# Optimization experiments

Hardware: AMD Instinct MI355X
Metric: run time of the kernel (lower is better)

Reference implementation:

```python
import jax, jax.numpy as jnp
import numpy as np

N_NODES = 50000
IN_CH = 128
OUT_CH = 64
N_EDGES = 800000
K_HOPS = 2


def setup_inputs() -> dict:
    key = jax.random.key(0)
    k1, k2, k3, k4 = jax.random.split(key, 4)
    x = jax.random.normal(k1, (N_NODES, IN_CH), dtype=jnp.float32)
    edge_index = jax.random.randint(k2, (2, N_EDGES), 0, N_NODES, dtype=jnp.int64)
    # SGC linear layer params (torch Linear default init approx)
    scale = 1.0 / np.sqrt(IN_CH)
    W = jax.random.uniform(k3, (IN_CH, OUT_CH), dtype=jnp.float32, minval=-scale, maxval=scale)
    b = jax.random.uniform(k4, (OUT_CH,), dtype=jnp.float32, minval=-scale, maxval=scale)
    return {"x": x, "edge_index": edge_index, "W": W, "b": b}


def _sgc_propagate(x, row, col, K):
    # GCN symmetric normalization with self-loops: S = D^-1/2 (A+I) D^-1/2
    n = x.shape[0]
    loop = jnp.arange(n, dtype=row.dtype)
    row = jnp.concatenate([row, loop])
    col = jnp.concatenate([col, loop])
    ones = jnp.ones(row.shape[0], dtype=x.dtype)
    deg = jax.ops.segment_sum(ones, col, num_segments=n)
    dinv = jnp.where(deg > 0, jax.lax.rsqrt(deg), 0.0)
    norm = dinv[row] * dinv[col]  # [E+N]
    for _ in range(K):
        # gather source features, weight, scatter-add to targets
        msg = norm[:, None] * x[row]  # [E+N, C]
        x = jax.ops.segment_sum(msg, col, num_segments=n)
    return x


def reference(x, edge_index, W, b):
    # Dropout is identity in eval mode (deterministic reference).
    row, col = edge_index[0], edge_index[1]
    h = _sgc_propagate(x, row, col, K_HOPS)  # [N, IN_CH]
    return h @ W + b  # [N, OUT_CH]
```

## Files before the change

kernel.cpp:

```cpp
#include <hip/hip_runtime.h>

#define N_NODES 50000
#define IN_CH   128
#define OUT_CH  64
#define N_EDGES 800000
#define NBINS   49
#define LBCAP   128
#define BINCAP  20000
#define PCAP    64
#define WT_STR  136


using short8  = __attribute__((ext_vector_type(8))) short;
using float4v = __attribute__((ext_vector_type(4))) float;

__device__ __forceinline__ unsigned int bpack(float a, float b) {
    unsigned int ua = __float_as_uint(a), ub = __float_as_uint(b);
    unsigned int ra = (ua + 0x7fffu + ((ua >> 16) & 1u)) >> 16;
    unsigned int rb = (ub + 0x7fffu + ((ub >> 16) & 1u)) & 0xffff0000u;
    return (ra & 0xffffu) | rb;
}

__global__ __launch_bounds__(256) void scatter_a(const int* __restrict__ row,
        const int* __restrict__ col, unsigned int* __restrict__ binbuf,
        int* __restrict__ gcur) {
    __shared__ unsigned int sbuf[NBINS][LBCAP];
    __shared__ int scnt[NBINS];
    __shared__ int sdst[NBINS];
    const int tid = threadIdx.x;
    for (int i = tid; i < NBINS; i += 256) scnt[i] = 0;
    __syncthreads();
    const int e0 = blockIdx.x * (N_EDGES / 256);
    for (int i = tid; i < N_EDGES / 256; i += 256) {
        int e = e0 + i;
        int s = row[e], t = col[e];
        int b = t >> 10;
        int pos = atomicAdd(&scnt[b], 1);
        if (pos < LBCAP)
            sbuf[b][pos] = ((unsigned)(t & 1023) << 16) | (unsigned)s;
    }
    __syncthreads();
    for (int b = tid; b < NBINS; b += 256) {
        int c = scnt[b]; if (c > LBCAP) c = LBCAP; scnt[b] = c;
        sdst[b] = atomicAdd(&gcur[b], c);
    }
    __syncthreads();
    for (int b = 0; b < NBINS; ++b) {
        int c = scnt[b], d = sdst[b];
        for (int i = tid; i < c; i += 256)
            binbuf[(size_t)b * BINCAP + d + i] = sbuf[b][i];
    }
}

__global__ __launch_bounds__(1024) void scatter_b(const unsigned int* __restrict__ binbuf,
        const int* __restrict__ gcur, unsigned short* __restrict__ esrc,
        unsigned char* __restrict__ fill8) {
    __shared__ int lcnt[1024];
    const int b  = blockIdx.x;
    const int t0 = b << 10;
    const int tid = threadIdx.x;
    lcnt[tid] = 0;
    __syncthreads();
    int cnt = gcur[b]; if (cnt > BINCAP) cnt = BINCAP;
    const unsigned int* src = binbuf + (size_t)b * BINCAP;
    for (int i = tid; i < cnt; i += 1024) {
        unsigned int e = src[i];
        int tl = e >> 16;
        int pos = atomicAdd(&lcnt[tl], 1);
        int t = t0 + tl;
        if (pos < PCAP && t < N_NODES)
            esrc[(size_t)pos * N_NODES + t] = (unsigned short)(e & 0xffffu);
    }
    __syncthreads();
    int t = t0 + tid;
    if (t < N_NODES) {
        int v = lcnt[tid]; if (v > PCAP) v = PCAP;
        fill8[t] = (unsigned char)v;
    }
}

__global__ __launch_bounds__(256) void gemm_mfma(const float* __restrict__ x,
        const float* __restrict__ W, float* __restrict__ y) {
    __shared__ unsigned short sWT[64 * WT_STR];
    const int tid = threadIdx.x;
    for (int i = tid; i < IN_CH * OUT_CH; i += 256) {
        int k = i >> 6, c = i & 63;
        unsigned int u = __float_as_uint(W[i]);
        u = (u + 0x7fffu + ((u >> 16) & 1u)) >> 16;
        sWT[c * WT_STR + k] = (unsigned short)u;
    }
    __syncthreads();
    const int lane = tid & 63;
    const int quad = lane >> 4;
    const int c15  = lane & 15;

    short8 bf[4][4];
    #pragma unroll
    for (int t = 0; t < 4; ++t)
        #pragma unroll
        for (int ch = 0; ch < 4; ++ch)
            bf[ch][t] = *(const short8*)&sWT[(t * 16 + c15) * WT_STR + ch * 32 + quad * 8];

    const int wave = (blockIdx.x * 256 + tid) >> 6;
    for (int tile = wave; tile < N_NODES / 16; tile += 1024) {
        const float* xr = x + ((size_t)tile * 16 + c15) * IN_CH;
        float4v acc[4] = {{0.f,0.f,0.f,0.f},{0.f,0.f,0.f,0.f},
                          {0.f,0.f,0.f,0.f},{0.f,0.f,0.f,0.f}};
        #pragma unroll
        for (int ch = 0; ch < 4; ++ch) {
            float4 f0 = *(const float4*)(xr + ch * 32 + quad * 8);
            float4 f1 = *(const float4*)(xr + ch * 32 + quad * 8 + 4);
            unsigned int d0 = bpack(f0.x, f0.y), d1 = bpack(f0.z, f0.w);
            unsigned int d2 = bpack(f1.x, f1.y), d3 = bpack(f1.z, f1.w);
            short8 a;
            a[0] = (short)d0; a[1] = (short)(d0 >> 16);
            a[2] = (short)d1; a[3] = (short)(d1 >> 16);
            a[4] = (short)d2; a[5] = (short)(d2 >> 16);
            a[6] = (short)d3; a[7] = (short)(d3 >> 16);
            #pragma unroll
            for (int t = 0; t < 4; ++t)
                acc[t] = __builtin_amdgcn_mfma_f32_16x16x32_bf16(a, bf[ch][t], acc[t], 0, 0, 0);
        }
        #pragma unroll
        for (int t = 0; t < 4; ++t)
            #pragma unroll
            for (int r = 0; r < 4; ++r)
                y[((size_t)tile * 16 + quad * 4 + r) * OUT_CH + t * 16 + c15] = acc[t][r];
    }
}

__global__ __launch_bounds__(256) void scale_z0(const float* __restrict__ y,
        const unsigned char* __restrict__ fill8, uint4* __restrict__ z0) {
    int gid = blockIdx.x * 256 + threadIdx.x;
    if (gid >= N_NODES * 8) return;
    int n = gid >> 3, q = gid & 7;
    float d = rsqrtf((float)((int)fill8[n] + 1));
    float4 a = ((const float4*)y)[n * 16 + q * 2];
    float4 b = ((const float4*)y)[n * 16 + q * 2 + 1];
    uint4 pk;
    pk.x = bpack(d * a.x, d * a.y);
    pk.y = bpack(d * a.z, d * a.w);
    pk.z = bpack(d * b.x, d * b.y);
    pk.w = bpack(d * b.z, d * b.w);
    z0[gid] = pk;
}

__global__ __launch_bounds__(256) void hop_gather(const uint4* __restrict__ hin,
        void* __restrict__ hout, const unsigned char* __restrict__ fill8,
        const unsigned short* __restrict__ esrc, const float* __restrict__ bias,
        int last) {
    int lane = threadIdx.x & 63;
    int g = lane >> 3;
    int q = lane & 7;
    int t = __builtin_amdgcn_readfirstlane(blockIdx.x * 4 + (threadIdx.x >> 6));
    if (t >= N_NODES) return;
    int deg = fill8[t];

    float acc[8] = {};
    if (g == 0) {
        uint4 r = hin[t * 8 + q];
        const unsigned int rw[4] = { r.x, r.y, r.z, r.w };
        #pragma unroll
        for (int j = 0; j < 4; ++j) {
            acc[2 * j]     = __uint_as_float(rw[j] << 16);
            acc[2 * j + 1] = __uint_as_float(rw[j] & 0xffff0000u);
        }
    }
    for (int base = 0; base < deg; base += 8) {
        int e = base + g;
        if (e < deg) {
            int s = (int)esrc[(size_t)e * N_NODES + t];
            uint4 r = hin[s * 8 + q];
            const unsigned int rw[4] = { r.x, r.y, r.z, r.w };
            #pragma unroll
            for (int j = 0; j < 4; ++j) {
                acc[2 * j]     += __uint_as_float(rw[j] << 16);
                acc[2 * j + 1] += __uint_as_float(rw[j] & 0xffff0000u);
            }
        }
    }
    #pragma unroll
    for (int j = 0; j < 8; ++j) {
        acc[j] += __shfl_xor(acc[j], 8);
        acc[j] += __shfl_xor(acc[j], 16);
        acc[j] += __shfl_xor(acc[j], 32);
    }
    if (g == 0) {
        if (!last) {
            float rdeg = 1.0f / (float)(deg + 1);
            uint4 pk;
            pk.x = bpack(acc[0] * rdeg, acc[1] * rdeg);
            pk.y = bpack(acc[2] * rdeg, acc[3] * rdeg);
            pk.z = bpack(acc[4] * rdeg, acc[5] * rdeg);
            pk.w = bpack(acc[6] * rdeg, acc[7] * rdeg);
            ((uint4*)hout)[t * 8 + q] = pk;
        } else {
            float d = rsqrtf((float)(deg + 1));
            float4 b0 = ((const float4*)bias)[q * 2];
            float4 b1 = ((const float4*)bias)[q * 2 + 1];
            float4 o0 = make_float4(d * acc[0] + b0.x, d * acc[1] + b0.y,
                                    d * acc[2] + b0.z, d * acc[3] + b0.w);
            float4 o1 = make_float4(d * acc[4] + b1.x, d * acc[5] + b1.y,
                                    d * acc[6] + b1.z, d * acc[7] + b1.w);
            ((float4*)hout)[t * 16 + q * 2]     = o0;
            ((float4*)hout)[t * 16 + q * 2 + 1] = o1;
        }
    }
}

extern "C" void kernel_launch(void* const* d_in, const int* in_sizes, int n_in,
                              void* d_out, int out_size, void* d_ws, size_t ws_size,
                              hipStream_t stream) {
    const float* x  = (const float*)d_in[0];
    const int*   ei = (const int*)d_in[1];
    const float* W  = (const float*)d_in[2];
    const float* b  = (const float*)d_in[3];
    float*       out = (float*)d_out;

    const int* row = ei;
    const int* col = ei + N_EDGES;

    char* ws = (char*)d_ws;
    size_t a = 0;
    auto alloc = [&](size_t bytes) { char* p = ws + a; a = (a + bytes + 255) & ~(size_t)255; return p; };
    int*            gcur   = (int*)           alloc(NBINS * sizeof(int));
    unsigned int*   binbuf = (unsigned int*)  alloc((size_t)NBINS * BINCAP * 4);
    unsigned short* esrc   = (unsigned short*)alloc((size_t)PCAP * N_NODES * 2);
    unsigned char*  fill8  = (unsigned char*) alloc(N_NODES);
    float*          y      = (float*)         alloc((size_t)N_NODES * OUT_CH * 4);
    unsigned int*   z0     = (unsigned int*)  alloc((size_t)N_NODES * OUT_CH * 2);
    unsigned int*   z1     = (unsigned int*)  alloc((size_t)N_NODES * OUT_CH * 2);

    hipMemsetAsync(gcur, 0, NBINS * sizeof(int), stream);

    const int B = 256;
    int gS = (N_NODES * 8 + B - 1) / B;
    int gH = (N_NODES + 3) / 4;

    scatter_a<<<256, B, 0, stream>>>(row, col, binbuf, gcur);
    scatter_b<<<NBINS, 1024, 0, stream>>>(binbuf, gcur, esrc, fill8);
    gemm_mfma<<<256, B, 0, stream>>>(x, W, y);
    scale_z0 <<<gS, B, 0, stream>>>(y, fill8, (uint4*)z0);
    hop_gather<<<gH, B, 0, stream>>>((const uint4*)z0, (void*)z1, fill8, esrc, b, 0);
    hop_gather<<<gH, B, 0, stream>>>((const uint4*)z1, (void*)out, fill8, esrc, b, 1);
}
```

Measured before the change: 183.5 us.

## Merge bin scatter and GEMM into one launch and widen edge binning grid

```diff
diff --git a/kernel.cpp b/kernel.cpp
--- a/kernel.cpp
+++ b/kernel.cpp
@@ -9,6 +9,10 @@
 #define BINCAP  20000
 #define PCAP    64
 #define WT_STR  136
+#define SA_B    500
+#define SA_E    1600
+#define SB_B    49
+#define GEMM_BL 196
 
 
 using short8  = __attribute__((ext_vector_type(8))) short;
@@ -28,62 +32,69 @@
     __shared__ int scnt[NBINS];
     __shared__ int sdst[NBINS];
     const int tid = threadIdx.x;
-    for (int i = tid; i < NBINS; i += 256) scnt[i] = 0;
-    __syncthreads();
-    const int e0 = blockIdx.x * (N_EDGES / 256);
-    for (int i = tid; i < N_EDGES / 256; i += 256) {
-        int e = e0 + i;
-        int s = row[e], t = col[e];
-        int b = t >> 10;
-        int pos = atomicAdd(&scnt[b], 1);
-        if (pos < LBCAP)
-            sbuf[b][pos] = ((unsigned)(t & 1023) << 16) | (unsigned)s;
-    }
-    __syncthreads();
-    for (int b = tid; b < NBINS; b += 256) {
-        int c = scnt[b]; if (c > LBCAP) c = LBCAP; scnt[b] = c;
-        sdst[b] = atomicAdd(&gcur[b], c);
-    }
-    __syncthreads();
-    for (int b = 0; b < NBINS; ++b) {
-        int c = scnt[b], d = sdst[b];
-        for (int i = tid; i < c; i += 256)
-            binbuf[(size_t)b * BINCAP + d + i] = sbuf[b][i];
-    }
-}
-
-__global__ __launch_bounds__(1024) void scatter_b(const unsigned int* __restrict__ binbuf,
-        const int* __restrict__ gcur, unsigned short* __restrict__ esrc,
-        unsigned char* __restrict__ fill8) {
-    __shared__ int lcnt[1024];
-    const int b  = blockIdx.x;
-    const int t0 = b << 10;
-    const int tid = threadIdx.x;
-    lcnt[tid] = 0;
-    __syncthreads();
-    int cnt = gcur[b]; if (cnt > BINCAP) cnt = BINCAP;
-    const unsigned int* src = binbuf + (size_t)b * BINCAP;
-    for (int i = tid; i < cnt; i += 1024) {
-        unsigned int e = src[i];
-        int tl = e >> 16;
-        int pos = atomicAdd(&lcnt[tl], 1);
-        int t = t0 + tl;
-        if (pos < PCAP && t < N_NODES)
-            esrc[(size_t)pos * N_NODES + t] = (unsigned short)(e & 0xffffu);
-    }
-    __syncthreads();
-    int t = t0 + tid;
-    if (t < N_NODES) {
-        int v = lcnt[tid]; if (v > PCAP) v = PCAP;
-        fill8[t] = (unsigned char)v;
-    }
-}
-
-__global__ __launch_bounds__(256) void gemm_mfma(const float* __restrict__ x,
-        const float* __restrict__ W, float* __restrict__ y) {
+    if (tid < NBINS) scnt[tid] = 0;
+    __syncthreads();
+    const int e0 = blockIdx.x * SA_E;
+    for (int i = tid; i < SA_E / 4; i += 256) {
+        int e = e0 + i * 4;
+        int4 t4 = *(const int4*)&col[e];
+        int4 s4 = *(const int4*)&row[e];
+        const int ts[4] = { t4.x, t4.y, t4.z, t4.w };
+        const int ss[4] = { s4.x, s4.y, s4.z, s4.w };
+        #pragma unroll
+        for (int j = 0; j < 4; ++j) {
+            int b = ts[j] >> 10;
+            int pos = atomicAdd(&scnt[b], 1);
+            if (pos < LBCAP)
+                sbuf[b][pos] = ((unsigned)(ts[j] & 1023) << 16) | (unsigned)ss[j];
+        }
+    }
+    __syncthreads();
+    if (tid < NBINS) {
+        int c = scnt[tid]; if (c > LBCAP) c = LBCAP; scnt[tid] = c;
+        sdst[tid] = atomicAdd(&gcur[tid], c);
+    }
+    __syncthreads();
+    const int wave = tid >> 6, lane = tid & 63;
+    for (int b = wave; b < NBINS; b += 4) {
+        int c = scnt[b];
+        size_t d = (size_t)b * BINCAP + sdst[b];
+        for (int i = lane; i < c; i += 64)
+            binbuf[d + i] = sbuf[b][i];
+    }
+}
+
+__global__ __launch_bounds__(1024) void scatb_gemm(
+        const unsigned int* __restrict__ binbuf, const int* __restrict__ gcur,
+        unsigned short* __restrict__ esrc, unsigned char* __restrict__ fill8,
+        const float* __restrict__ x, const float* __restrict__ W,
+        float* __restrict__ y) {
+    const int bid = blockIdx.x, tid = threadIdx.x;
+    if (bid < SB_B) {
+        __shared__ int lcnt[1024];
+        const int t0 = bid << 10;
+        lcnt[tid] = 0;
+        __syncthreads();
+        int cnt = gcur[bid]; if (cnt > BINCAP) cnt = BINCAP;
+        const unsigned int* src = binbuf + (size_t)bid * BINCAP;
+        for (int i = tid; i < cnt; i += 1024) {
+            unsigned int e = src[i];
+            int tl = e >> 16;
+            int pos = atomicAdd(&lcnt[tl], 1);
+            int t = t0 + tl;
+            if (pos < PCAP && t < N_NODES)
+                esrc[(size_t)pos * N_NODES + t] = (unsigned short)(e & 0xffffu);
+        }
+        __syncthreads();
+        int t = t0 + tid;
+        if (t < N_NODES) {
+            int v = lcnt[tid]; if (v > PCAP) v = PCAP;
+            fill8[t] = (unsigned char)v;
+        }
+        return;
+    }
     __shared__ unsigned short sWT[64 * WT_STR];
-    const int tid = threadIdx.x;
-    for (int i = tid; i < IN_CH * OUT_CH; i += 256) {
+    for (int i = tid; i < IN_CH * OUT_CH; i += 1024) {
         int k = i >> 6, c = i & 63;
         unsigned int u = __float_as_uint(W[i]);
         u = (u + 0x7fffu + ((u >> 16) & 1u)) >> 16;
@@ -93,6 +104,8 @@
     const int lane = tid & 63;
     const int quad = lane >> 4;
     const int c15  = lane & 15;
+    const int tile = (bid - SB_B) * 16 + (tid >> 6);
+    if (tile >= N_NODES / 16) return;
 
     short8 bf[4][4];
     #pragma unroll
@@ -101,32 +114,29 @@
         for (int ch = 0; ch < 4; ++ch)
             bf[ch][t] = *(const short8*)&sWT[(t * 16 + c15) * WT_STR + ch * 32 + quad * 8];
 
-    const int wave = (blockIdx.x * 256 + tid) >> 6;
-    for (int tile = wave; tile < N_NODES / 16; tile += 1024) {
-        const float* xr = x + ((size_t)tile * 16 + c15) * IN_CH;
-        float4v acc[4] = {{0.f,0.f,0.f,0.f},{0.f,0.f,0.f,0.f},
-                          {0.f,0.f,0.f,0.f},{0.f,0.f,0.f,0.f}};
-        #pragma unroll
-        for (int ch = 0; ch < 4; ++ch) {
-            float4 f0 = *(const float4*)(xr + ch * 32 + quad * 8);
-            float4 f1 = *(const float4*)(xr + ch * 32 + quad * 8 + 4);
-            unsigned int d0 = bpack(f0.x, f0.y), d1 = bpack(f0.z, f0.w);
-            unsigned int d2 = bpack(f1.x, f1.y), d3 = bpack(f1.z, f1.w);
-            short8 a;
-            a[0] = (short)d0; a[1] = (short)(d0 >> 16);
-            a[2] = (short)d1; a[3] = (short)(d1 >> 16);
-            a[4] = (short)d2; a[5] = (short)(d2 >> 16);
-            a[6] = (short)d3; a[7] = (short)(d3 >> 16);
-            #pragma unroll
-            for (int t = 0; t < 4; ++t)
-                acc[t] = __builtin_amdgcn_mfma_f32_16x16x32_bf16(a, bf[ch][t], acc[t], 0, 0, 0);
-        }
+    const float* xr = x + ((size_t)tile * 16 + c15) * IN_CH;
+    float4v acc[4] = {{0.f,0.f,0.f,0.f},{0.f,0.f,0.f,0.f},
+                      {0.f,0.f,0.f,0.f},{0.f,0.f,0.f,0.f}};
+    #pragma unroll
+    for (int ch = 0; ch < 4; ++ch) {
+        float4 f0 = *(const float4*)(xr + ch * 32 + quad * 8);
+        float4 f1 = *(const float4*)(xr + ch * 32 + quad * 8 + 4);
+        unsigned int d0 = bpack(f0.x, f0.y), d1 = bpack(f0.z, f0.w);
+        unsigned int d2 = bpack(f1.x, f1.y), d3 = bpack(f1.z, f1.w);
+        short8 a8;
+        a8[0] = (short)d0; a8[1] = (short)(d0 >> 16);
+        a8[2] = (short)d1; a8[3] = (short)(d1 >> 16);
+        a8[4] = (short)d2; a8[5] = (short)(d2 >> 16);
+        a8[6] = (short)d3; a8[7] = (short)(d3 >> 16);
         #pragma unroll
         for (int t = 0; t < 4; ++t)
-            #pragma unroll
-            for (int r = 0; r < 4; ++r)
-                y[((size_t)tile * 16 + quad * 4 + r) * OUT_CH + t * 16 + c15] = acc[t][r];
-    }
+            acc[t] = __builtin_amdgcn_mfma_f32_16x16x32_bf16(a8, bf[ch][t], acc[t], 0, 0, 0);
+    }
+    #pragma unroll
+    for (int t = 0; t < 4; ++t)
+        #pragma unroll
+        for (int r = 0; r < 4; ++r)
+            y[((size_t)tile * 16 + quad * 4 + r) * OUT_CH + t * 16 + c15] = acc[t][r];
 }
 
 __global__ __launch_bounds__(256) void scale_z0(const float* __restrict__ y,
@@ -237,9 +247,8 @@
     int gS = (N_NODES * 8 + B - 1) / B;
     int gH = (N_NODES + 3) / 4;
 
-    scatter_a<<<256, B, 0, stream>>>(row, col, binbuf, gcur);
-    scatter_b<<<NBINS, 1024, 0, stream>>>(binbuf, gcur, esrc, fill8);
-    gemm_mfma<<<256, B, 0, stream>>>(x, W, y);
+    scatter_a<<<SA_B, B, 0, stream>>>(row, col, binbuf, gcur);
+    scatb_gemm<<<SB_B + GEMM_BL, 1024, 0, stream>>>(binbuf, gcur, esrc, fill8, x, W, y);
     scale_z0 <<<gS, B, 0, stream>>>(y, fill8, (uint4*)z0);
     hop_gather<<<gH, B, 0, stream>>>((const uint4*)z0, (void*)z1, fill8, esrc, b, 0);
     hop_gather<<<gH, B, 0, stream>>>((const uint4*)z1, (void*)out, fill8, esrc, b, 1);
```

Result: faster. 165.8 us (-9.7%).
